# Kernel optimization log

Hardware: AMD Instinct MI355X
Metric: run time of the kernel (lower is better)

The kernel has to match this reference:

```python
import jax, jax.numpy as jnp
import numpy as np

N = 100_000          # ent_num
D = 256              # ent_dim
E_RAND = 3_200_000   # random edges (avg degree 32); + N self loops
NEG_SLOPE = 0.2      # LeakyReLU slope used by SpGraphAttentionLayer


def setup_inputs() -> dict:
    key = jax.random.key(0)
    k0, k1, k2, k3, k4, k5 = jax.random.split(key, 6)
    edges_rand = jax.random.randint(k0, (2, E_RAND), 0, N, dtype=jnp.int32)
    self_loops = jnp.tile(jnp.arange(N, dtype=jnp.int32)[None, :], (2, 1))
    edges = jnp.concatenate([edges_rand, self_loops], axis=1)  # [2, E]
    scale_w = 1.0 / np.sqrt(D).astype(np.float32)
    scale_a = 0.1 / np.sqrt(D).astype(np.float32)
    emb = jax.random.normal(k1, (N, D), jnp.float32)
    W1 = jax.random.normal(k2, (D, D), jnp.float32) * scale_w
    a1 = jax.random.normal(k3, (2 * D,), jnp.float32) * scale_a
    W2 = jax.random.normal(k4, (D, D), jnp.float32) * scale_w
    a2 = jax.random.normal(k5, (2 * D,), jnp.float32) * scale_a
    return {"emb": emb, "W1": W1, "a1": a1, "W2": W2, "a2": a2, "edges": edges}


def gat_layer(h, W, a, src, dst):
    # h: [N, D] node features; edges (src -> aggregates from dst)
    h2 = h @ W                              # [N, D]
    s_src = h2 @ a[:D]                      # [N] contribution of a . h_src
    s_dst = h2 @ a[D:]                      # [N] contribution of a . h_dst
    score = s_src[src] + s_dst[dst]         # [E] = a . [h_src; h_dst]
    e = jnp.exp(-jax.nn.leaky_relu(score, NEG_SLOPE))  # [E], pyGAT sparse form
    denom = jax.ops.segment_sum(e, src, num_segments=h.shape[0])          # [N]
    num = jax.ops.segment_sum(e[:, None] * h2[dst], src,
                              num_segments=h.shape[0])                    # [N, D]
    return jax.nn.elu(num / denom[:, None])


def reference(emb, W1, a1, W2, a2, edges):
    src, dst = edges[0], edges[1]
    h = gat_layer(emb, W1, a1, src, dst)
    h = gat_layer(h, W2, a2, src, dst)
    return h
```

## Files before the change

kernel.cpp:

```cpp
#include <hip/hip_runtime.h>
#include <hip/hip_bf16.h>

#define D 256
#define NEG_SLOPE 0.2f
#define BM 128
#define BN 128
#define BK 64
#define LDK 72
#define SCAN_CHUNK 1024

using bf16x8 = __attribute__((ext_vector_type(8))) __bf16;
using f32x4  = __attribute__((ext_vector_type(4))) float;

__device__ __forceinline__ float bf2f(unsigned short u) {
    return __uint_as_float(((unsigned int)u) << 16);
}
__device__ __forceinline__ unsigned short f2bf(float f) {
    unsigned int u = __float_as_uint(f);
    unsigned int r = (u + 0x7FFF + ((u >> 16) & 1)) >> 16;
    return (unsigned short)r;
}


__global__ void transW_kernel(const float* __restrict__ W, unsigned short* __restrict__ WT) {
    const int k = blockIdx.x, n = threadIdx.x;
    WT[(size_t)n * D + k] = f2bf(W[(size_t)k * D + n]);
}


__global__ void count_kernel(const int* __restrict__ src, int* __restrict__ counts, int E) {
    int t = blockIdx.x * blockDim.x + threadIdx.x;
    if (t < E) atomicAdd(&counts[src[t]], 1);
}

__global__ __launch_bounds__(256) void scan_partial_kernel(
    const int* __restrict__ counts, int* __restrict__ partial, int n)
{
    __shared__ int ws[4];
    const int tid = threadIdx.x;
    const int lane = tid & 63, wv = tid >> 6;
    const int idx = blockIdx.x * SCAN_CHUNK + tid * 4;
    int4 v = make_int4(0, 0, 0, 0);
    if (idx + 3 < n) v = *(const int4*)(counts + idx);
    else {
        if (idx + 0 < n) v.x = counts[idx + 0];
        if (idx + 1 < n) v.y = counts[idx + 1];
        if (idx + 2 < n) v.z = counts[idx + 2];
        if (idx + 3 < n) v.w = counts[idx + 3];
    }
    int s = v.x + v.y + v.z + v.w;
    #pragma unroll
    for (int off = 32; off > 0; off >>= 1) s += __shfl_xor(s, off);
    if (lane == 0) ws[wv] = s;
    __syncthreads();
    if (tid == 0) partial[blockIdx.x] = ws[0] + ws[1] + ws[2] + ws[3];
}

__global__ __launch_bounds__(128) void scan_chunks_kernel(
    const int* __restrict__ partial, int* __restrict__ chunkoff,
    int* __restrict__ row_ptr, int nchunks, int n)
{
    __shared__ int sm[128];
    const int tid = threadIdx.x;
    const int v = (tid < nchunks) ? partial[tid] : 0;
    sm[tid] = v;
    __syncthreads();
    #pragma unroll
    for (int off = 1; off < 128; off <<= 1) {
        int t = (tid >= off) ? sm[tid - off] : 0;
        __syncthreads();
        sm[tid] += t;
        __syncthreads();
    }
    if (tid < nchunks) chunkoff[tid] = sm[tid] - v;
    if (tid == 127) row_ptr[n] = sm[127];
}

__global__ __launch_bounds__(256) void scan_write_kernel(
    const int* __restrict__ counts, const int* __restrict__ chunkoff,
    int* __restrict__ row_ptr, int n)
{
    __shared__ int wsum[4];
    const int tid = threadIdx.x;
    const int lane = tid & 63, wv = tid >> 6;
    const int idx = blockIdx.x * SCAN_CHUNK + tid * 4;
    int4 v = make_int4(0, 0, 0, 0);
    if (idx + 3 < n) v = *(const int4*)(counts + idx);
    else {
        if (idx + 0 < n) v.x = counts[idx + 0];
        if (idx + 1 < n) v.y = counts[idx + 1];
        if (idx + 2 < n) v.z = counts[idx + 2];
        if (idx + 3 < n) v.w = counts[idx + 3];
    }
    const int s = v.x + v.y + v.z + v.w;
    int x = s;
    #pragma unroll
    for (int off = 1; off < 64; off <<= 1) {
        int t = __shfl_up(x, off);
        if (lane >= off) x += t;
    }
    if (lane == 63) wsum[wv] = x;
    __syncthreads();
    int wo = chunkoff[blockIdx.x];
    for (int w = 0; w < 4; ++w) if (w < wv) wo += wsum[w];
    int excl = wo + x - s;
    if (idx + 0 < n) row_ptr[idx + 0] = excl;
    if (idx + 1 < n) row_ptr[idx + 1] = excl + v.x;
    if (idx + 2 < n) row_ptr[idx + 2] = excl + v.x + v.y;
    if (idx + 3 < n) row_ptr[idx + 3] = excl + v.x + v.y + v.z;
}

__global__ void fill_kernel(const int* __restrict__ src, const int* __restrict__ dst,
                            const int* __restrict__ row_ptr, int* __restrict__ fillp,
                            int* __restrict__ col, int E) {
    int t = blockIdx.x * blockDim.x + threadIdx.x;
    if (t < E) {
        int s = src[t];
        int pos = atomicAdd(&fillp[s], 1);
        col[row_ptr[s] + pos] = dst[t];
    }
}


__global__ __launch_bounds__(256) void gemm_mfma(
    const unsigned short* __restrict__ Ab, const float* __restrict__ Af,
    const unsigned short* __restrict__ BT,
    unsigned short* __restrict__ C, int M)
{
    __shared__ unsigned short smem[2 * BM * LDK];
    unsigned short* As_ = smem;
    unsigned short* Bs_ = smem + BM * LDK;
    const int tid = threadIdx.x;
    const int m0 = blockIdx.x * BM;
    const int n0 = blockIdx.y * BN;
    const int lane = tid & 63;
    const int wv = tid >> 6;
    const int wm = (wv & 1) * 64;
    const int wn = (wv >> 1) * 64;
    const int l15 = lane & 15;
    const int quad = lane >> 4;

    f32x4 acc[4][4];
    #pragma unroll
    for (int i = 0; i < 4; ++i)
        #pragma unroll
        for (int j = 0; j < 4; ++j)
            acc[i][j] = (f32x4){0.f, 0.f, 0.f, 0.f};

    for (int k0 = 0; k0 < D; k0 += BK) {
        #pragma unroll
        for (int c = tid; c < BM * 8; c += 256) {
            const int row = c >> 3, j = c & 7;
            const int gr = m0 + row;
            uint4 av = make_uint4(0, 0, 0, 0);
            if (gr < M) {
                if (Af) {
                    const float* p = Af + (size_t)gr * D + k0 + j * 8;
                    const float4 f0 = *(const float4*)p;
                    const float4 f1 = *(const float4*)(p + 4);
                    av.x = (unsigned int)f2bf(f0.x) | ((unsigned int)f2bf(f0.y) << 16);
                    av.y = (unsigned int)f2bf(f0.z) | ((unsigned int)f2bf(f0.w) << 16);
                    av.z = (unsigned int)f2bf(f1.x) | ((unsigned int)f2bf(f1.y) << 16);
                    av.w = (unsigned int)f2bf(f1.z) | ((unsigned int)f2bf(f1.w) << 16);
                } else {
                    av = *(const uint4*)(Ab + (size_t)gr * D + k0 + j * 8);
                }
            }
            *(uint4*)(As_ + row * LDK + j * 8) = av;
            const uint4 bv = *(const uint4*)(BT + (size_t)(n0 + row) * D + k0 + j * 8);
            *(uint4*)(Bs_ + row * LDK + j * 8) = bv;
        }
        __syncthreads();
        #pragma unroll
        for (int s = 0; s < 2; ++s) {
            bf16x8 af[4], bfr[4];
            #pragma unroll
            for (int i = 0; i < 4; ++i)
                af[i] = *(const bf16x8*)(As_ + (wm + i * 16 + l15) * LDK + s * 32 + quad * 8);
            #pragma unroll
            for (int j = 0; j < 4; ++j)
                bfr[j] = *(const bf16x8*)(Bs_ + (wn + j * 16 + l15) * LDK + s * 32 + quad * 8);
            #pragma unroll
            for (int i = 0; i < 4; ++i)
                #pragma unroll
                for (int j = 0; j < 4; ++j)
                    acc[i][j] = __builtin_amdgcn_mfma_f32_16x16x32_bf16(
                        af[i], bfr[j], acc[i][j], 0, 0, 0);
        }
        __syncthreads();
    }

    unsigned short* Cw = smem + wv * (64 * LDK);
    #pragma unroll
    for (int i = 0; i < 4; ++i)
        #pragma unroll
        for (int j = 0; j < 4; ++j)
            #pragma unroll
            for (int r = 0; r < 4; ++r)
                Cw[(i * 16 + quad * 4 + r) * LDK + j * 16 + l15] = f2bf(acc[i][j][r]);
    __syncthreads();
    #pragma unroll
    for (int rr = 0; rr < 64; rr += 2) {
        const int row = rr + (lane >> 5);
        const unsigned int wd = *(const unsigned int*)(Cw + row * LDK + (lane & 31) * 2);
        const int gr = m0 + wm + row;
        if (gr < M)
            *(unsigned int*)(C + (size_t)gr * D + n0 + wn + (lane & 31) * 2) = wd;
    }
}


__global__ __launch_bounds__(256) void score_kernel(
    const unsigned short* __restrict__ h2, const float* __restrict__ a,
    float* __restrict__ s_src, float* __restrict__ s_dst, int Nn)
{
    const int lane = threadIdx.x & 63;
    const int w = threadIdx.x >> 6;
    const int row = blockIdx.x * 4 + w;
    if (row >= Nn) return;
    const ushort4 h = *(const ushort4*)(h2 + (size_t)row * D + lane * 4);
    const float4 a1v = *(const float4*)(a + lane * 4);
    const float4 a2v = *(const float4*)(a + D + lane * 4);
    const float hx = bf2f(h.x), hy = bf2f(h.y), hz = bf2f(h.z), hw = bf2f(h.w);
    float p1 = hx * a1v.x + hy * a1v.y + hz * a1v.z + hw * a1v.w;
    float p2 = hx * a2v.x + hy * a2v.y + hz * a2v.z + hw * a2v.w;
    #pragma unroll
    for (int off = 32; off > 0; off >>= 1) {
        p1 += __shfl_down(p1, off);
        p2 += __shfl_down(p2, off);
    }
    if (lane == 0) { s_src[row] = p1; s_dst[row] = p2; }
}


__global__ __launch_bounds__(256) void agg_kernel(
    const unsigned short* __restrict__ h2, const float* __restrict__ s_src,
    const float* __restrict__ s_dst, const int* __restrict__ row_ptr,
    const int* __restrict__ col, unsigned short* __restrict__ out_bf16,
    float* __restrict__ out_f32, int Nn)
{
    const int lane = threadIdx.x & 63;
    const int half = lane >> 5;
    const int hl = lane & 31;
    const int node = blockIdx.x * 4 + (threadIdx.x >> 6);
    if (node >= Nn) return;
    const int beg = row_ptr[node], end = row_ptr[node + 1];
    const float ssrc = s_src[node];
    const unsigned short* hp = h2 + hl * 8;

    float a[8];
    #pragma unroll
    for (int i = 0; i < 8; ++i) a[i] = 0.f;
    float dpart = 0.f;

    for (int c0 = beg; c0 < end; c0 += 64) {
        const int cnt = min(64, end - c0);
        int j = 0;
        float e = 0.f;
        if (lane < cnt) {
            j = col[c0 + lane];
            const float sc = ssrc + s_dst[j];
            const float l = sc >= 0.f ? sc : NEG_SLOPE * sc;
            e = __expf(-l);
        }
        dpart += e;
        for (int k = 0; k < cnt; k += 8) {
            const int   j0 = __shfl(j, k + 0 + half);
            const int   j1 = __shfl(j, k + 2 + half);
            const int   j2 = __shfl(j, k + 4 + half);
            const int   j3 = __shfl(j, k + 6 + half);
            const float e0 = __shfl(e, k + 0 + half);
            const float e1 = __shfl(e, k + 2 + half);
            const float e2 = __shfl(e, k + 4 + half);
            const float e3 = __shfl(e, k + 6 + half);
            const uint4 u0 = *(const uint4*)(hp + (size_t)j0 * D);
            const uint4 u1 = *(const uint4*)(hp + (size_t)j1 * D);
            const uint4 u2 = *(const uint4*)(hp + (size_t)j2 * D);
            const uint4 u3 = *(const uint4*)(hp + (size_t)j3 * D);
            #define ACC8(u, ev)                                               \
                a[0] = fmaf(ev, __uint_as_float((u).x << 16), a[0]);          \
                a[1] = fmaf(ev, __uint_as_float((u).x & 0xffff0000u), a[1]);  \
                a[2] = fmaf(ev, __uint_as_float((u).y << 16), a[2]);          \
                a[3] = fmaf(ev, __uint_as_float((u).y & 0xffff0000u), a[3]);  \
                a[4] = fmaf(ev, __uint_as_float((u).z << 16), a[4]);          \
                a[5] = fmaf(ev, __uint_as_float((u).z & 0xffff0000u), a[5]);  \
                a[6] = fmaf(ev, __uint_as_float((u).w << 16), a[6]);          \
                a[7] = fmaf(ev, __uint_as_float((u).w & 0xffff0000u), a[7]);
            ACC8(u0, e0)
            ACC8(u1, e1)
            ACC8(u2, e2)
            ACC8(u3, e3)
            #undef ACC8
        }
    }

    #pragma unroll
    for (int i = 0; i < 8; ++i) a[i] += __shfl_xor(a[i], 32);

    float denom = dpart;
    #pragma unroll
    for (int off = 32; off > 0; off >>= 1) denom += __shfl_xor(denom, off);
    const float inv = 1.f / denom;

    if (half == 0) {
        float v[8];
        #pragma unroll
        for (int i = 0; i < 8; ++i) {
            const float x = a[i] * inv;
            v[i] = x > 0.f ? x : expm1f(x);
        }
        if (out_bf16) {
            uint4 o;
            o.x = (unsigned int)f2bf(v[0]) | ((unsigned int)f2bf(v[1]) << 16);
            o.y = (unsigned int)f2bf(v[2]) | ((unsigned int)f2bf(v[3]) << 16);
            o.z = (unsigned int)f2bf(v[4]) | ((unsigned int)f2bf(v[5]) << 16);
            o.w = (unsigned int)f2bf(v[6]) | ((unsigned int)f2bf(v[7]) << 16);
            *(uint4*)(out_bf16 + (size_t)node * D + hl * 8) = o;
        } else {
            float* p = out_f32 + (size_t)node * D + hl * 8;
            *(float4*)(p)     = make_float4(v[0], v[1], v[2], v[3]);
            *(float4*)(p + 4) = make_float4(v[4], v[5], v[6], v[7]);
        }
    }
}


static inline size_t align_up(size_t x, size_t a) { return (x + a - 1) & ~(a - 1); }

extern "C" void kernel_launch(void* const* d_in, const int* in_sizes, int n_in,
                              void* d_out, int out_size, void* d_ws, size_t ws_size,
                              hipStream_t stream)
{
    const float* emb = (const float*)d_in[0];
    const float* W1  = (const float*)d_in[1];
    const float* a1  = (const float*)d_in[2];
    const float* W2  = (const float*)d_in[3];
    const float* a2  = (const float*)d_in[4];
    const int* edges = (const int*)d_in[5];
    const int Nn = in_sizes[0] / D;
    const int E  = in_sizes[5] / 2;
    const int* src = edges;
    const int* dst = edges + E;
    const int nchunks = (Nn + SCAN_CHUNK - 1) / SCAN_CHUNK;

    size_t off = 0;
    char* base = (char*)d_ws;
    unsigned short* hA = (unsigned short*)(base + off);
    off = align_up(off + (size_t)Nn * D * sizeof(unsigned short), 256);
    unsigned short* hB = (unsigned short*)(base + off);
    off = align_up(off + (size_t)Nn * D * sizeof(unsigned short), 256);
    unsigned short* WT1 = (unsigned short*)(base + off);
    off = align_up(off + (size_t)D * D * sizeof(unsigned short), 256);
    unsigned short* WT2 = (unsigned short*)(base + off);
    off = align_up(off + (size_t)D * D * sizeof(unsigned short), 256);
    float* s_src = (float*)(base + off); off = align_up(off + (size_t)Nn * sizeof(float), 256);
    float* s_dst = (float*)(base + off); off = align_up(off + (size_t)Nn * sizeof(float), 256);
    int* row_ptr = (int*)(base + off);   off = align_up(off + (size_t)(Nn + 1) * sizeof(int), 256);
    const size_t cstride = align_up((size_t)Nn * sizeof(int), 256);
    int* counts  = (int*)(base + off);   off += cstride;
    int* fillp   = (int*)(base + off);   off += cstride;
    int* partial = (int*)(base + off);   off = align_up(off + (size_t)nchunks * sizeof(int), 256);
    int* chunkoff= (int*)(base + off);   off = align_up(off + (size_t)nchunks * sizeof(int), 256);
    int* col     = (int*)(base + off);   off = align_up(off + (size_t)E * sizeof(int), 256);

    transW_kernel<<<D, D, 0, stream>>>(W1, WT1);
    transW_kernel<<<D, D, 0, stream>>>(W2, WT2);

    hipMemsetAsync(counts, 0, 2 * cstride, stream);
    count_kernel<<<(E + 255) / 256, 256, 0, stream>>>(src, counts, E);
    scan_partial_kernel<<<nchunks, 256, 0, stream>>>(counts, partial, Nn);
    scan_chunks_kernel<<<1, 128, 0, stream>>>(partial, chunkoff, row_ptr, nchunks, Nn);
    scan_write_kernel<<<nchunks, 256, 0, stream>>>(counts, chunkoff, row_ptr, Nn);
    fill_kernel<<<(E + 255) / 256, 256, 0, stream>>>(src, dst, row_ptr, fillp, col, E);

    dim3 ggrid((Nn + BM - 1) / BM, D / BN);
    gemm_mfma<<<ggrid, 256, 0, stream>>>(nullptr, emb, WT1, hA, Nn);
    score_kernel<<<(Nn + 3) / 4, 256, 0, stream>>>(hA, a1, s_src, s_dst, Nn);
    agg_kernel<<<(Nn + 3) / 4, 256, 0, stream>>>(hA, s_src, s_dst, row_ptr, col, hB, nullptr, Nn);
    gemm_mfma<<<ggrid, 256, 0, stream>>>(hB, nullptr, WT2, hA, Nn);
    score_kernel<<<(Nn + 3) / 4, 256, 0, stream>>>(hA, a2, s_src, s_dst, Nn);
    agg_kernel<<<(Nn + 3) / 4, 256, 0, stream>>>(hA, s_src, s_dst, row_ptr, col, nullptr,
                                                 (float*)d_out, Nn);
}
```

Before: 1.040 ms.

## Fuse score into GEMM epilogue, merge prep/scan kernels, nontemporal stores

The attention score dot products are now computed in the GEMM epilogue from the bf16 tile and accumulated into per-layer score buffers with atomics, which removes the separate score kernels and their re-read of h2. The weight transposes and the workspace zeroing are merged into one prep kernel. The three-pass scan is replaced by a single-block scan, and the aggregation output uses nontemporal stores. This cuts launch count and memory traffic, but adds float atomics (two contributions per row, so ordering can vary) and serialises the scan onto one workgroup.

Result: slower. 1.087 ms (+4.5%).

```diff
diff --git a/kernel.cpp b/kernel.cpp
--- a/kernel.cpp
+++ b/kernel.cpp
@@ -7,10 +7,10 @@
 #define BN 128
 #define BK 64
 #define LDK 72
-#define SCAN_CHUNK 1024
 
 using bf16x8 = __attribute__((ext_vector_type(8))) __bf16;
 using f32x4  = __attribute__((ext_vector_type(4))) float;
+using u32x4  = __attribute__((ext_vector_type(4))) unsigned int;
 
 __device__ __forceinline__ float bf2f(unsigned short u) {
     return __uint_as_float(((unsigned int)u) << 16);
@@ -22,9 +22,21 @@
 }
 
 
-__global__ void transW_kernel(const float* __restrict__ W, unsigned short* __restrict__ WT) {
-    const int k = blockIdx.x, n = threadIdx.x;
-    WT[(size_t)n * D + k] = f2bf(W[(size_t)k * D + n]);
+__global__ __launch_bounds__(256) void prep_kernel(
+    const float* __restrict__ W1, const float* __restrict__ W2,
+    unsigned short* __restrict__ WT1, unsigned short* __restrict__ WT2,
+    int4* __restrict__ zbase, int nz16)
+{
+    const int b = blockIdx.x, tid = threadIdx.x;
+    if (b < 256) {
+        WT1[(size_t)tid * D + b] = f2bf(W1[(size_t)b * D + tid]);
+    } else if (b < 512) {
+        const int k = b - 256;
+        WT2[(size_t)tid * D + k] = f2bf(W2[(size_t)k * D + tid]);
+    } else {
+        const int w = (b - 512) * 256 + tid;
+        if (w < nz16) zbase[w] = make_int4(0, 0, 0, 0);
+    }
 }
 
 
@@ -33,81 +45,47 @@
     if (t < E) atomicAdd(&counts[src[t]], 1);
 }
 
-__global__ __launch_bounds__(256) void scan_partial_kernel(
-    const int* __restrict__ counts, int* __restrict__ partial, int n)
-{
-    __shared__ int ws[4];
+__global__ __launch_bounds__(1024) void scan_all_kernel(
+    const int* __restrict__ counts, int* __restrict__ row_ptr, int n)
+{
+    __shared__ int ws[16];
     const int tid = threadIdx.x;
     const int lane = tid & 63, wv = tid >> 6;
-    const int idx = blockIdx.x * SCAN_CHUNK + tid * 4;
-    int4 v = make_int4(0, 0, 0, 0);
-    if (idx + 3 < n) v = *(const int4*)(counts + idx);
-    else {
-        if (idx + 0 < n) v.x = counts[idx + 0];
-        if (idx + 1 < n) v.y = counts[idx + 1];
-        if (idx + 2 < n) v.z = counts[idx + 2];
-        if (idx + 3 < n) v.w = counts[idx + 3];
-    }
-    int s = v.x + v.y + v.z + v.w;
-    #pragma unroll
-    for (int off = 32; off > 0; off >>= 1) s += __shfl_xor(s, off);
-    if (lane == 0) ws[wv] = s;
-    __syncthreads();
-    if (tid == 0) partial[blockIdx.x] = ws[0] + ws[1] + ws[2] + ws[3];
-}
-
-__global__ __launch_bounds__(128) void scan_chunks_kernel(
-    const int* __restrict__ partial, int* __restrict__ chunkoff,
-    int* __restrict__ row_ptr, int nchunks, int n)
-{
-    __shared__ int sm[128];
-    const int tid = threadIdx.x;
-    const int v = (tid < nchunks) ? partial[tid] : 0;
-    sm[tid] = v;
-    __syncthreads();
-    #pragma unroll
-    for (int off = 1; off < 128; off <<= 1) {
-        int t = (tid >= off) ? sm[tid - off] : 0;
+    int base = 0;
+    for (int c0 = 0; c0 < n; c0 += 4096) {
+        const int idx = c0 + tid * 4;
+        int4 v = make_int4(0, 0, 0, 0);
+        if (idx + 3 < n) v = *(const int4*)(counts + idx);
+        else {
+            if (idx + 0 < n) v.x = counts[idx + 0];
+            if (idx + 1 < n) v.y = counts[idx + 1];
+            if (idx + 2 < n) v.z = counts[idx + 2];
+            if (idx + 3 < n) v.w = counts[idx + 3];
+        }
+        const int s = v.x + v.y + v.z + v.w;
+        int x = s;
+        #pragma unroll
+        for (int off = 1; off < 64; off <<= 1) {
+            int t = __shfl_up(x, off);
+            if (lane >= off) x += t;
+        }
+        if (lane == 63) ws[wv] = x;
         __syncthreads();
-        sm[tid] += t;
+        int wo = base;
+        #pragma unroll
+        for (int w = 0; w < 16; ++w) if (w < wv) wo += ws[w];
+        const int excl = wo + x - s;
+        if (idx + 0 < n) row_ptr[idx + 0] = excl;
+        if (idx + 1 < n) row_ptr[idx + 1] = excl + v.x;
+        if (idx + 2 < n) row_ptr[idx + 2] = excl + v.x + v.y;
+        if (idx + 3 < n) row_ptr[idx + 3] = excl + v.x + v.y + v.z;
+        int tot = 0;
+        #pragma unroll
+        for (int w = 0; w < 16; ++w) tot += ws[w];
         __syncthreads();
-    }
-    if (tid < nchunks) chunkoff[tid] = sm[tid] - v;
-    if (tid == 127) row_ptr[n] = sm[127];
-}
-
-__global__ __launch_bounds__(256) void scan_write_kernel(
-    const int* __restrict__ counts, const int* __restrict__ chunkoff,
-    int* __restrict__ row_ptr, int n)
-{
-    __shared__ int wsum[4];
-    const int tid = threadIdx.x;
-    const int lane = tid & 63, wv = tid >> 6;
-    const int idx = blockIdx.x * SCAN_CHUNK + tid * 4;
-    int4 v = make_int4(0, 0, 0, 0);
-    if (idx + 3 < n) v = *(const int4*)(counts + idx);
-    else {
-        if (idx + 0 < n) v.x = counts[idx + 0];
-        if (idx + 1 < n) v.y = counts[idx + 1];
-        if (idx + 2 < n) v.z = counts[idx + 2];
-        if (idx + 3 < n) v.w = counts[idx + 3];
-    }
-    const int s = v.x + v.y + v.z + v.w;
-    int x = s;
-    #pragma unroll
-    for (int off = 1; off < 64; off <<= 1) {
-        int t = __shfl_up(x, off);
-        if (lane >= off) x += t;
-    }
-    if (lane == 63) wsum[wv] = x;
-    __syncthreads();
-    int wo = chunkoff[blockIdx.x];
-    for (int w = 0; w < 4; ++w) if (w < wv) wo += wsum[w];
-    int excl = wo + x - s;
-    if (idx + 0 < n) row_ptr[idx + 0] = excl;
-    if (idx + 1 < n) row_ptr[idx + 1] = excl + v.x;
-    if (idx + 2 < n) row_ptr[idx + 2] = excl + v.x + v.y;
-    if (idx + 3 < n) row_ptr[idx + 3] = excl + v.x + v.y + v.z;
+        base += tot;
+    }
+    if (tid == 0) row_ptr[n] = base;
 }
 
 __global__ void fill_kernel(const int* __restrict__ src, const int* __restrict__ dst,
@@ -125,7 +103,8 @@
 __global__ __launch_bounds__(256) void gemm_mfma(
     const unsigned short* __restrict__ Ab, const float* __restrict__ Af,
     const unsigned short* __restrict__ BT,
-    unsigned short* __restrict__ C, int M)
+    unsigned short* __restrict__ C, int M,
+    const float* __restrict__ av, float* __restrict__ s_src, float* __restrict__ s_dst)
 {
     __shared__ unsigned short smem[2 * BM * LDK];
     unsigned short* As_ = smem;
@@ -152,21 +131,21 @@
         for (int c = tid; c < BM * 8; c += 256) {
             const int row = c >> 3, j = c & 7;
             const int gr = m0 + row;
-            uint4 av = make_uint4(0, 0, 0, 0);
+            uint4 avv = make_uint4(0, 0, 0, 0);
             if (gr < M) {
                 if (Af) {
                     const float* p = Af + (size_t)gr * D + k0 + j * 8;
                     const float4 f0 = *(const float4*)p;
                     const float4 f1 = *(const float4*)(p + 4);
-                    av.x = (unsigned int)f2bf(f0.x) | ((unsigned int)f2bf(f0.y) << 16);
-                    av.y = (unsigned int)f2bf(f0.z) | ((unsigned int)f2bf(f0.w) << 16);
-                    av.z = (unsigned int)f2bf(f1.x) | ((unsigned int)f2bf(f1.y) << 16);
-                    av.w = (unsigned int)f2bf(f1.z) | ((unsigned int)f2bf(f1.w) << 16);
+                    avv.x = (unsigned int)f2bf(f0.x) | ((unsigned int)f2bf(f0.y) << 16);
+                    avv.y = (unsigned int)f2bf(f0.z) | ((unsigned int)f2bf(f0.w) << 16);
+                    avv.z = (unsigned int)f2bf(f1.x) | ((unsigned int)f2bf(f1.y) << 16);
+                    avv.w = (unsigned int)f2bf(f1.z) | ((unsigned int)f2bf(f1.w) << 16);
                 } else {
-                    av = *(const uint4*)(Ab + (size_t)gr * D + k0 + j * 8);
+                    avv = *(const uint4*)(Ab + (size_t)gr * D + k0 + j * 8);
                 }
             }
-            *(uint4*)(As_ + row * LDK + j * 8) = av;
+            *(uint4*)(As_ + row * LDK + j * 8) = avv;
             const uint4 bv = *(const uint4*)(BT + (size_t)(n0 + row) * D + k0 + j * 8);
             *(uint4*)(Bs_ + row * LDK + j * 8) = bv;
         }
@@ -199,37 +178,30 @@
             for (int r = 0; r < 4; ++r)
                 Cw[(i * 16 + quad * 4 + r) * LDK + j * 16 + l15] = f2bf(acc[i][j][r]);
     __syncthreads();
+    const int ccol = n0 + wn + (lane & 31) * 2;
+    const float a1c0 = av[ccol],     a1c1 = av[ccol + 1];
+    const float a2c0 = av[D + ccol], a2c1 = av[D + ccol + 1];
     #pragma unroll
     for (int rr = 0; rr < 64; rr += 2) {
         const int row = rr + (lane >> 5);
         const unsigned int wd = *(const unsigned int*)(Cw + row * LDK + (lane & 31) * 2);
         const int gr = m0 + wm + row;
         if (gr < M)
-            *(unsigned int*)(C + (size_t)gr * D + n0 + wn + (lane & 31) * 2) = wd;
-    }
-}
-
-
-__global__ __launch_bounds__(256) void score_kernel(
-    const unsigned short* __restrict__ h2, const float* __restrict__ a,
-    float* __restrict__ s_src, float* __restrict__ s_dst, int Nn)
-{
-    const int lane = threadIdx.x & 63;
-    const int w = threadIdx.x >> 6;
-    const int row = blockIdx.x * 4 + w;
-    if (row >= Nn) return;
-    const ushort4 h = *(const ushort4*)(h2 + (size_t)row * D + lane * 4);
-    const float4 a1v = *(const float4*)(a + lane * 4);
-    const float4 a2v = *(const float4*)(a + D + lane * 4);
-    const float hx = bf2f(h.x), hy = bf2f(h.y), hz = bf2f(h.z), hw = bf2f(h.w);
-    float p1 = hx * a1v.x + hy * a1v.y + hz * a1v.z + hw * a1v.w;
-    float p2 = hx * a2v.x + hy * a2v.y + hz * a2v.z + hw * a2v.w;
-    #pragma unroll
-    for (int off = 32; off > 0; off >>= 1) {
-        p1 += __shfl_down(p1, off);
-        p2 += __shfl_down(p2, off);
-    }
-    if (lane == 0) { s_src[row] = p1; s_dst[row] = p2; }
+            *(unsigned int*)(C + (size_t)gr * D + ccol) = wd;
+        const float f0 = bf2f((unsigned short)(wd & 0xffffu));
+        const float f1 = bf2f((unsigned short)(wd >> 16));
+        float p1 = f0 * a1c0 + f1 * a1c1;
+        float p2 = f0 * a2c0 + f1 * a2c1;
+        #pragma unroll
+        for (int off = 16; off > 0; off >>= 1) {
+            p1 += __shfl_xor(p1, off);
+            p2 += __shfl_xor(p2, off);
+        }
+        if ((lane & 31) == 0 && gr < M) {
+            atomicAdd(&s_src[gr], p1);
+            atomicAdd(&s_dst[gr], p2);
+        }
+    }
 }
 
 
@@ -310,16 +282,18 @@
             v[i] = x > 0.f ? x : expm1f(x);
         }
         if (out_bf16) {
-            uint4 o;
+            u32x4 o;
             o.x = (unsigned int)f2bf(v[0]) | ((unsigned int)f2bf(v[1]) << 16);
             o.y = (unsigned int)f2bf(v[2]) | ((unsigned int)f2bf(v[3]) << 16);
             o.z = (unsigned int)f2bf(v[4]) | ((unsigned int)f2bf(v[5]) << 16);
             o.w = (unsigned int)f2bf(v[6]) | ((unsigned int)f2bf(v[7]) << 16);
-            *(uint4*)(out_bf16 + (size_t)node * D + hl * 8) = o;
+            __builtin_nontemporal_store(o, (u32x4*)(out_bf16 + (size_t)node * D + hl * 8));
         } else {
             float* p = out_f32 + (size_t)node * D + hl * 8;
-            *(float4*)(p)     = make_float4(v[0], v[1], v[2], v[3]);
-            *(float4*)(p + 4) = make_float4(v[4], v[5], v[6], v[7]);
+            f32x4 o0 = {v[0], v[1], v[2], v[3]};
+            f32x4 o1 = {v[4], v[5], v[6], v[7]};
+            __builtin_nontemporal_store(o0, (f32x4*)p);
+            __builtin_nontemporal_store(o1, (f32x4*)(p + 4));
         }
     }
 }
@@ -341,7 +315,6 @@
     const int E  = in_sizes[5] / 2;
     const int* src = edges;
     const int* dst = edges + E;
-    const int nchunks = (Nn + SCAN_CHUNK - 1) / SCAN_CHUNK;
 
     size_t off = 0;
     char* base = (char*)d_ws;
@@ -353,32 +326,33 @@
     off = align_up(off + (size_t)D * D * sizeof(unsigned short), 256);
     unsigned short* WT2 = (unsigned short*)(base + off);
     off = align_up(off + (size_t)D * D * sizeof(unsigned short), 256);
-    float* s_src = (float*)(base + off); off = align_up(off + (size_t)Nn * sizeof(float), 256);
-    float* s_dst = (float*)(base + off); off = align_up(off + (size_t)Nn * sizeof(float), 256);
-    int* row_ptr = (int*)(base + off);   off = align_up(off + (size_t)(Nn + 1) * sizeof(int), 256);
+
     const size_t cstride = align_up((size_t)Nn * sizeof(int), 256);
+    char* zstart = base + off;
+    float* s1s = (float*)(base + off); off += (size_t)Nn * sizeof(float);
+    float* s1d = (float*)(base + off); off += (size_t)Nn * sizeof(float);
+    float* s2s = (float*)(base + off); off += (size_t)Nn * sizeof(float);
+    float* s2d = (float*)(base + off); off += (size_t)Nn * sizeof(float);
+    off = align_up(off, 256);
     int* counts  = (int*)(base + off);   off += cstride;
     int* fillp   = (int*)(base + off);   off += cstride;
-    int* partial = (int*)(base + off);   off = align_up(off + (size_t)nchunks * sizeof(int), 256);
-    int* chunkoff= (int*)(base + off);   off = align_up(off + (size_t)nchunks * sizeof(int), 256);
+    const size_t zbytes = (size_t)(base + off - zstart);
+    const int nz16 = (int)(zbytes / 16);
+
+    int* row_ptr = (int*)(base + off);   off = align_up(off + (size_t)(Nn + 1) * sizeof(int), 256);
     int* col     = (int*)(base + off);   off = align_up(off + (size_t)E * sizeof(int), 256);
 
-    transW_kernel<<<D, D, 0, stream>>>(W1, WT1);
-    transW_kernel<<<D, D, 0, stream>>>(W2, WT2);
-
-    hipMemsetAsync(counts, 0, 2 * cstride, stream);
+    const int zblocks = (nz16 + 255) / 256;
+    prep_kernel<<<512 + zblocks, 256, 0, stream>>>(W1, W2, WT1, WT2, (int4*)zstart, nz16);
+
     count_kernel<<<(E + 255) / 256, 256, 0, stream>>>(src, counts, E);
-    scan_partial_kernel<<<nchunks, 256, 0, stream>>>(counts, partial, Nn);
-    scan_chunks_kernel<<<1, 128, 0, stream>>>(partial, chunkoff, row_ptr, nchunks, Nn);
-    scan_write_kernel<<<nchunks, 256, 0, stream>>>(counts, chunkoff, row_ptr, Nn);
+    scan_all_kernel<<<1, 1024, 0, stream>>>(counts, row_ptr, Nn);
     fill_kernel<<<(E + 255) / 256, 256, 0, stream>>>(src, dst, row_ptr, fillp, col, E);
 
     dim3 ggrid((Nn + BM - 1) / BM, D / BN);
-    gemm_mfma<<<ggrid, 256, 0, stream>>>(nullptr, emb, WT1, hA, Nn);
-    score_kernel<<<(Nn + 3) / 4, 256, 0, stream>>>(hA, a1, s_src, s_dst, Nn);
-    agg_kernel<<<(Nn + 3) / 4, 256, 0, stream>>>(hA, s_src, s_dst, row_ptr, col, hB, nullptr, Nn);
-    gemm_mfma<<<ggrid, 256, 0, stream>>>(hB, nullptr, WT2, hA, Nn);
-    score_kernel<<<(Nn + 3) / 4, 256, 0, stream>>>(hA, a2, s_src, s_dst, Nn);
-    agg_kernel<<<(Nn + 3) / 4, 256, 0, stream>>>(hA, s_src, s_dst, row_ptr, col, nullptr,
+    gemm_mfma<<<ggrid, 256, 0, stream>>>(nullptr, emb, WT1, hA, Nn, a1, s1s, s1d);
+    agg_kernel<<<(Nn + 3) / 4, 256, 0, stream>>>(hA, s1s, s1d, row_ptr, col, hB, nullptr, Nn);
+    gemm_mfma<<<ggrid, 256, 0, stream>>>(hB, nullptr, WT2, hA, Nn, a2, s2s, s2d);
+    agg_kernel<<<(Nn + 3) / 4, 256, 0, stream>>>(hA, s2s, s2d, row_ptr, col, nullptr,
                                                  (float*)d_out, Nn);
 }
```
